# Kernel optimization log

Measured on AMD Instinct MI355X. Metric: run time of the kernel, lower is better.

Reference implementation:

```python
import jax, jax.numpy as jnp
import numpy as np

VOCAB = 100000
EMBED = 256
HIDDEN = 256
HOPS = 3
NHEAD = 4
SEQEND = 2
B, MEM, SEN, QLEN = 32, 50, 20, 20


def setup_inputs() -> dict:
    key = jax.random.key(0)
    ks = jax.random.split(key, 24)

    def lin(k, o, i):
        return jax.random.normal(k, (o, i), jnp.float32) * (1.0 / np.sqrt(i))

    story = jax.random.randint(ks[0], (B, MEM, SEN), 3, VOCAB, dtype=jnp.int32)
    pos_s = jax.random.randint(ks[1], (B, MEM), 0, SEN, dtype=jnp.int32)
    story = jnp.where(jnp.arange(SEN)[None, None, :] == pos_s[..., None], SEQEND, story)
    query = jax.random.randint(ks[2], (B, QLEN), 3, VOCAB, dtype=jnp.int32)
    pos_q = jax.random.randint(ks[3], (B,), 0, QLEN, dtype=jnp.int32)
    query = jnp.where(jnp.arange(QLEN)[None, :] == pos_q[:, None], SEQEND, query)

    embed = jax.random.normal(ks[4], (VOCAB, EMBED), jnp.float32) * 0.05
    embed = embed.at[0].set(0.0)  # padding_idx=0
    H = HIDDEN
    params = dict(
        embed=embed,
        w_ih=lin(ks[5], 3 * H, EMBED), w_hh=lin(ks[6], 3 * H, H),
        b_ih=jnp.zeros((3 * H,), jnp.float32), b_hh=jnp.zeros((3 * H,), jnp.float32),
        ft_w1=lin(ks[7], H, H), ft_b1=jnp.zeros((H,), jnp.float32),
        ft_w2=lin(ks[8], H, H), ft_b2=jnp.zeros((H,), jnp.float32),
        wq=lin(ks[9], H, H), bq=jnp.zeros((H,), jnp.float32),
        wk=lin(ks[10], H, H), bk=jnp.zeros((H,), jnp.float32),
        wv=lin(ks[11], H, H), bv=jnp.zeros((H,), jnp.float32),
        wo=lin(ks[12], H, H), bo=jnp.zeros((H,), jnp.float32),
        g_w1=lin(ks[13], 3 * H, 3 * H), g_b1=jnp.zeros((3 * H,), jnp.float32),
        g_w2=lin(ks[14], 3 * H, 3 * H), g_b2=jnp.zeros((3 * H,), jnp.float32),
        v_w=lin(ks[15], VOCAB, 3 * H),
    )
    return dict(story=story, query=query, **params)


def _gru(x, h0, w_ih, w_hh, b_ih, b_hh):
    # x: [N, T, E], h0: [N, H] -> outputs [N, T, H], final h [N, H]
    def step(h, xt):
        gi = xt @ w_ih.T + b_ih
        gh = h @ w_hh.T + b_hh
        i_r, i_z, i_n = jnp.split(gi, 3, axis=-1)
        h_r, h_z, h_n = jnp.split(gh, 3, axis=-1)
        r = jax.nn.sigmoid(i_r + h_r)
        z = jax.nn.sigmoid(i_z + h_z)
        n = jnp.tanh(i_n + r * h_n)
        h_new = (1.0 - z) * n + z * h
        return h_new, h_new
    h_f, ys = jax.lax.scan(step, h0, jnp.swapaxes(x, 0, 1))
    return jnp.swapaxes(ys, 0, 1), h_f


def _seqend_idx(tokens):
    # first index of SEQEND along last axis, else last position
    is_end = tokens == SEQEND
    idx = jnp.argmax(is_end, axis=-1)
    return jnp.where(is_end.any(axis=-1), idx, tokens.shape[-1] - 1)


def reference(story, query, embed, w_ih, w_hh, b_ih, b_hh, ft_w1, ft_b1, ft_w2, ft_b2,
              wq, bq, wk, bk, wv, bv, wo, bo, g_w1, g_b1, g_w2, g_b2, v_w):
    H, nh = HIDDEN, NHEAD
    dk = H // nh

    def f_t(x):
        return jax.nn.relu(x @ ft_w1.T + ft_b1) @ ft_w2.T + ft_b2

    # --- story encoding: GRU hidden carried ACROSS batch elements (as in torch loop) ---
    story_embs = embed[story]  # [B, MEM, SEN, E]
    def story_step(h, emb_b):
        outs, h_f = _gru(emb_b, h, w_ih, w_hh, b_ih, b_hh)  # [MEM, SEN, H]
        return h_f, outs
    h0 = jnp.zeros((story.shape[1], H), story_embs.dtype)
    _, story_outs = jax.lax.scan(story_step, h0, story_embs)  # [B, MEM, SEN, H]

    s_idx = _seqend_idx(story)  # [B, MEM]
    memory_slots = jnp.take_along_axis(story_outs, s_idx[..., None, None], axis=2)[:, :, 0, :]  # [B, MEM, H]

    # --- query encoding ---
    q_embs = embed[query]  # [B, QLEN, E]
    q_outs, _ = _gru(q_embs, jnp.zeros((query.shape[0], H), q_embs.dtype), w_ih, w_hh, b_ih, b_hh)
    q_idx = _seqend_idx(query)  # [B]
    real_query = jnp.take_along_axis(q_outs, q_idx[:, None, None], axis=1)[:, 0, :]  # [B, H]

    # --- multi-hop attention ---
    def mha(qv, mem):
        b, m, _ = mem.shape
        q = (qv @ wq.T + bq).reshape(b, nh, dk)
        k = (mem @ wk.T + bk).reshape(b, m, nh, dk).transpose(0, 2, 1, 3)
        v = (mem @ wv.T + bv).reshape(b, m, nh, dk).transpose(0, 2, 1, 3)
        scores = jnp.einsum('bhmd,bhd->bhm', k, q) / jnp.sqrt(jnp.float32(dk))
        a = jax.nn.softmax(scores, axis=-1)
        out = jnp.einsum('bhm,bhmd->bhd', a, v).reshape(b, H)
        return out @ wo.T + bo

    o_k = f_t(real_query)
    buffers = []
    for _ in range(HOPS):
        mb = mha(o_k, memory_slots)
        buffers.append(mb)
        o_k = f_t(mb)
    memory_buffers = jnp.stack(buffers, axis=1)  # [B, HOPS, H]

    # --- ReasonModule: pairwise MLP over hops ---
    b, K, _ = memory_buffers.shape
    left = jnp.broadcast_to(memory_buffers[:, None, :, :], (b, K, K, H)).reshape(b, K * K, H)
    right = jnp.broadcast_to(memory_buffers[:, :, None, :], (b, K, K, H)).reshape(b, K * K, H)
    qx = jnp.broadcast_to(real_query[:, None, :], (b, K * K, H))
    combined = jnp.concatenate([left, right, qx], axis=-1)  # [B, K*K, 3H]
    t = jax.nn.relu(combined @ g_w1.T + g_b1) @ g_w2.T + g_b2
    reasoning = jax.nn.relu(t).sum(axis=1)  # [B, 3H]

    return reasoning @ v_w.T  # [B, VOCAB]
```

## Files before the change

kernel.cpp:

```cpp
#include <hip/hip_runtime.h>


#define TPB 256
#define NB    32
#define MEMN  50
#define SEN   20
#define VOC   100000
#define SEQEND_TOK 2
#define NGRU  82
#define NTILE 1530

#define GI_OFF    0
#define KVB_OFF   0
#define MB_OFF    819200
#define T1_OFF    843776
#define T2_OFF    1064960
#define RS_OFF    1286144
#define WTIH_OFF  25067520
#define WTHH_OFF  25264128
#define KVT_OFF   25460736
#define WQT_OFF   25591808
#define WOT_OFF   25657344
#define F1T_OFF   25722880
#define F2T_OFF   25788416
#define G1T_OFF   25853952
#define G2T_OFF   26443776
#define BKV_OFF   27033600
#define IDX_OFF   27034112
#define SLOT_OFF  27035744
#define RQ_OFF    27445344
#define CNT_OFF   27453536

__global__ void k_setup(const float* __restrict__ w_ih, const float* __restrict__ w_hh,
                        const float* __restrict__ wk,  const float* __restrict__ wv,
                        const float* __restrict__ wq,  const float* __restrict__ wo,
                        const float* __restrict__ f1,  const float* __restrict__ f2,
                        const float* __restrict__ g1,  const float* __restrict__ g2,
                        const float* __restrict__ bk,  const float* __restrict__ bv,
                        const int* __restrict__ story, const int* __restrict__ query,
                        float* __restrict__ ws)
{
  int g = blockIdx.x * TPB + threadIdx.x;
  if (g < 196608) { int j = g >> 8, k = g & 255; ws[WTIH_OFF + k*768 + j] = w_ih[g]; return; }
  g -= 196608;
  if (g < 196608) { int j = g >> 8, k = g & 255; ws[WTHH_OFF + k*768 + j] = w_hh[g]; return; }
  g -= 196608;
  if (g < 65536) { int j = g >> 8, k = g & 255; ws[KVT_OFF + k*512 + j] = wk[g]; return; }
  g -= 65536;
  if (g < 65536) { int j = g >> 8, k = g & 255; ws[KVT_OFF + k*512 + 256 + j] = wv[g]; return; }
  g -= 65536;
  if (g < 65536) { int j = g >> 8, k = g & 255; ws[WQT_OFF + k*256 + j] = wq[g]; return; }
  g -= 65536;
  if (g < 65536) { int j = g >> 8, k = g & 255; ws[WOT_OFF + k*256 + j] = wo[g]; return; }
  g -= 65536;
  if (g < 65536) { int j = g >> 8, k = g & 255; ws[F1T_OFF + k*256 + j] = f1[g]; return; }
  g -= 65536;
  if (g < 65536) { int j = g >> 8, k = g & 255; ws[F2T_OFF + k*256 + j] = f2[g]; return; }
  g -= 65536;
  if (g < 589824) { int j = g / 768, k = g - j*768; ws[G1T_OFF + k*768 + j] = g1[g]; return; }
  g -= 589824;
  if (g < 589824) { int j = g / 768, k = g - j*768; ws[G2T_OFF + k*768 + j] = g2[g]; return; }
  g -= 589824;
  if (g < 512) { ws[BKV_OFF + g] = (g < 256) ? bk[g] : bv[g - 256]; return; }
  g -= 512;
  if (g < 1600) {
    const int* st = story + g * SEN;
    int idx = SEN - 1;
    for (int t = 0; t < SEN; ++t) { if (st[t] == SEQEND_TOK) { idx = t; break; } }
    ((int*)(ws + IDX_OFF))[g] = idx;
    return;
  }
  g -= 1600;
  if (g < 32) {
    const int* qt = query + g * SEN;
    int idx = SEN - 1;
    for (int t = 0; t < SEN; ++t) { if (qt[t] == SEQEND_TOK) { idx = t; break; } }
    ((int*)(ws + IDX_OFF))[1600 + g] = idx;
    return;
  }
  g -= 32;
  if (g < 33) ((unsigned int*)(ws + CNT_OFF))[g] = 0u;
}

__global__ __launch_bounds__(1024, 1) void k_fused(
    float* __restrict__ gi,
    const float* __restrict__ w_hh, const float* __restrict__ b_hh,
    const int* __restrict__ idxI,
    const float* __restrict__ wihT, const float* __restrict__ b_ih,
    const int* __restrict__ tokS, const int* __restrict__ tokQ,
    const float* __restrict__ embed,
    float* __restrict__ slot_out, float* __restrict__ rq_out,
    unsigned int* __restrict__ cnt)
{
  __shared__ __align__(16) char smem[114688];
  const int bid = blockIdx.x;
  const int tid = threadIdx.x;

  if (bid >= NGRU) {
    float* At = (float*)smem;
    float* Bt = At + 4224;
    const int tix = bid - NGRU;
    const int mt = tix / 6, nt = tix - mt * 6;
    const int m0 = mt * 128, n0 = nt * 128;
    const int tx = tid & 15, ty = (tid >> 4) & 63;
    float acc[2][8] = {};

    for (int k0 = 0; k0 < 256; k0 += 32) {
      for (int idx = tid; idx < 4096; idx += 1024) {
        int r = idx >> 5, kk = idx & 31;
        int row = m0 + r;
        int tok = (row < 32000) ? tokS[row] : tokQ[row - 32000];
        At[r * 33 + kk] = embed[(size_t)tok * 256 + k0 + kk];
      }
      for (int idx = tid; idx < 4096; idx += 1024) {
        int jj = idx & 127, kk = idx >> 7;
        Bt[jj * 33 + kk] = wihT[(k0 + kk) * 768 + n0 + jj];
      }
      __syncthreads();
#pragma unroll
      for (int kk = 0; kk < 32; ++kk) {
        float a0 = At[ty * 33 + kk], a1 = At[(64 + ty) * 33 + kk];
        float bb[8];
#pragma unroll
        for (int i = 0; i < 8; ++i) bb[i] = Bt[(i * 16 + tx) * 33 + kk];
#pragma unroll
        for (int i = 0; i < 8; ++i) { acc[0][i] += a0 * bb[i]; acc[1][i] += a1 * bb[i]; }
      }
      __syncthreads();
    }
#pragma unroll
    for (int i = 0; i < 2; ++i) {
      int row = m0 + i * 64 + ty;
#pragma unroll
      for (int j2 = 0; j2 < 8; ++j2) {
        int col = n0 + j2 * 16 + tx;
        gi[(size_t)row * 768 + col] = acc[i][j2] + b_ih[col];
      }
    }
    __threadfence();
    __syncthreads();
    if (tid == 0) {
      const int rLo = m0, rHi = m0 + 127;
      const int cLo = (rLo < 32000) ? (rLo / 1000) : 32;
      const int cHi = (rHi < 32000) ? (rHi / 1000) : 32;
      __hip_atomic_fetch_add(&cnt[cLo], 1u, __ATOMIC_RELEASE, __HIP_MEMORY_SCOPE_AGENT);
      if (cHi != cLo)
        __hip_atomic_fetch_add(&cnt[cHi], 1u, __ATOMIC_RELEASE, __HIP_MEMORY_SCOPE_AGENT);
    }
    return;
  }

  const int mode = (bid >= MEMN) ? 1 : 0;
  const int blk = mode ? (bid - MEMN) : bid;
  float* __restrict__ cap_out = mode ? rq_out : slot_out;

  float* tot   = (float*)smem;
  float* ptail = tot + 768;
  float* hs    = ptail + 768;

  float4 w4[48];
  if (tid < 768) {
    const float* wrow = w_hh + (size_t)tid * 256;
#pragma unroll
    for (int q = 0; q < 48; ++q) w4[q] = ((const float4*)wrow)[q];
  } else {
    const int u = tid - 768;
#pragma unroll
    for (int rr = 0; rr < 3; ++rr) {
      const float* wrow = w_hh + (size_t)(u + rr * 256) * 256 + 192;
#pragma unroll
      for (int q = 0; q < 16; ++q) w4[rr * 16 + q] = ((const float4*)wrow)[q];
    }
  }
  const float bh = (tid < 768) ? b_hh[tid] : 0.f;

  if (tid < 256) hs[tid] = 0.f;
  float hold = 0.f;
  __syncthreads();

  const int steps = mode ? SEN : (NB * SEN);
  int b = 0, t = 0, cs = 0;

#pragma unroll 1
  for (int s = 0; s < steps; ++s) {
    if (t == 0) {
      if (tid == 0) {
        const int c   = mode ? 32 : b;
        const int rLo = mode ? 32000 : b * 1000;
        const int rHi = mode ? 32639 : b * 1000 + 999;
        const unsigned expv = 6u * (unsigned)(rHi / 128 - rLo / 128 + 1);
        while (__hip_atomic_load(&cnt[c], __ATOMIC_ACQUIRE, __HIP_MEMORY_SCOPE_AGENT) < expv)
          __builtin_amdgcn_s_sleep(16);
      }
      __syncthreads();
      cs = idxI[mode ? (1600 + blk) : (b * MEMN + blk)];
    }
    const int srow = mode ? (32000 + blk * SEN + t) : (b * 1000 + blk * SEN + t);

    if (tid < 768) {
      float dot = 0.f;
#pragma unroll
      for (int q = 0; q < 48; ++q) {
        float4 h4 = ((const float4*)hs)[q];
        dot += w4[q].x * h4.x + w4[q].y * h4.y + w4[q].z * h4.z + w4[q].w * h4.w;
      }
      float v = dot + bh;
      if (tid < 512) v += gi[(size_t)srow * 768 + tid];
      tot[tid] = v;
    } else {
      const int u = tid - 768;
      float p0 = 0.f, p1 = 0.f, p2 = 0.f;
      const float4* ht = (const float4*)(hs + 192);
#pragma unroll
      for (int q = 0; q < 16; ++q) {
        float4 h4 = ht[q];
        p0 += w4[q     ].x * h4.x + w4[q     ].y * h4.y + w4[q     ].z * h4.z + w4[q     ].w * h4.w;
        p1 += w4[16 + q].x * h4.x + w4[16 + q].y * h4.y + w4[16 + q].z * h4.z + w4[16 + q].w * h4.w;
        p2 += w4[32 + q].x * h4.x + w4[32 + q].y * h4.y + w4[32 + q].z * h4.z + w4[32 + q].w * h4.w;
      }
      ptail[u] = p0; ptail[u + 256] = p1; ptail[u + 512] = p2;
    }
    __syncthreads();

    if (tid < 256) {
      float Sr = tot[tid]       + ptail[tid];
      float Sz = tot[tid + 256] + ptail[tid + 256];
      float Sn = tot[tid + 512] + ptail[tid + 512];
      float gn = gi[(size_t)srow * 768 + 512 + tid];
      float rg = 1.f / (1.f + __expf(-Sr));
      float zg = 1.f / (1.f + __expf(-Sz));
      float xn = gn + rg * Sn;
      xn = fminf(fmaxf(xn, -15.f), 15.f);
      float e2 = __expf(-2.f * xn);
      float ng = (1.f - e2) / (1.f + e2);
      float hnew = (1.f - zg) * ng + zg * hold;
      hs[tid] = hnew;
      if (t == cs) cap_out[(mode ? blk : (b * MEMN + blk)) * 256 + tid] = hnew;
      hold = hnew;
    }
    __syncthreads();
    if (++t == SEN) { t = 0; ++b; }
  }
}

template<int MODE, int BM>
__global__ __launch_bounds__(256) void k_gemm(
    const float* __restrict__ A, const float* __restrict__ B,
    const float* __restrict__ bias, float* __restrict__ C,
    int M, int N, int K, int relu,
    const float* __restrict__ mbp, const float* __restrict__ rqp)
{
  __shared__ float At[BM * 33];
  __shared__ float Bt[128 * 33];
  constexpr int R = BM / 16;
  const int m0 = blockIdx.x * BM, n0 = blockIdx.y * 128;
  const int tx = threadIdx.x & 15, ty = threadIdx.x >> 4;
  float acc[R][8] = {};

  for (int k0 = 0; k0 < K; k0 += 32) {
    for (int idx = threadIdx.x; idx < BM * 32; idx += 256) {
      int r = idx >> 5, kk = idx & 31;
      int row = m0 + r, kg = k0 + kk;
      float v = 0.f;
      if (MODE == 2) {
        if (row < 288) {
          int b = row / 9, p = row - b * 9;
          v = (kg < 256) ? mbp[(b*3 + (p % 3))*256 + kg]
            : (kg < 512) ? mbp[(b*3 + (p / 3))*256 + (kg - 256)]
                         : rqp[b*256 + (kg - 512)];
        }
      } else {
        if (row < M) v = A[(size_t)row * K + kg];
      }
      At[r * 33 + kk] = v;
    }
    for (int idx = threadIdx.x; idx < 4096; idx += 256) {
      int jj = idx & 127, kk = idx >> 7;
      Bt[jj * 33 + kk] = B[(k0 + kk) * N + n0 + jj];
    }
    __syncthreads();
#pragma unroll
    for (int kk = 0; kk < 32; ++kk) {
      float a[R], bb[8];
#pragma unroll
      for (int i = 0; i < R; ++i) a[i] = At[(i * 16 + ty) * 33 + kk];
#pragma unroll
      for (int i = 0; i < 8; ++i) bb[i] = Bt[(i * 16 + tx) * 33 + kk];
#pragma unroll
      for (int i = 0; i < R; ++i)
#pragma unroll
        for (int j2 = 0; j2 < 8; ++j2) acc[i][j2] += a[i] * bb[j2];
    }
    __syncthreads();
  }
#pragma unroll
  for (int i = 0; i < R; ++i) {
    int row = m0 + i * 16 + ty;
    if (row >= M) continue;
#pragma unroll
    for (int j2 = 0; j2 < 8; ++j2) {
      int col = n0 + j2 * 16 + tx;
      float v = acc[i][j2] + bias[col];
      if (relu) v = fmaxf(v, 0.f);
      C[(size_t)row * N + col] = v;
    }
  }
}

__device__ __forceinline__ float gemv256(const float* __restrict__ WT,
                                         const float* __restrict__ xs, int j)
{
  float acc = 0.f;
#pragma unroll 64
  for (int k = 0; k < 256; ++k) acc += xs[k] * WT[k * 256 + j];
  return acc;
}

__global__ __launch_bounds__(256) void k_hops(
    const float* __restrict__ rq, const float* __restrict__ kvb,
    const float* __restrict__ wqT, const float* __restrict__ bq,
    const float* __restrict__ woT, const float* __restrict__ bo,
    const float* __restrict__ f1T, const float* __restrict__ fb1,
    const float* __restrict__ f2T, const float* __restrict__ fb2,
    float* __restrict__ mb)
{
  const int b = blockIdx.x, j = threadIdx.x;
  __shared__ float lk[50 * 259];
  __shared__ float lv[50 * 259];
  __shared__ float xs[256], tb[256], qs[256], avs[256], ob[256], asc[256];

  for (int idx = j; idx < 12800; idx += 256) {
    int m = idx >> 8, d = idx & 255;
    lk[m * 259 + d] = kvb[(b * MEMN + m) * 512 + d];
    lv[m * 259 + d] = kvb[(b * MEMN + m) * 512 + 256 + d];
  }
  xs[j] = rq[b * 256 + j];
  __syncthreads();

  float v = fmaxf(gemv256(f1T, xs, j) + fb1[j], 0.f);
  __syncthreads(); tb[j] = v; __syncthreads();
  v = gemv256(f2T, tb, j) + fb2[j];
  __syncthreads(); xs[j] = v; __syncthreads();

  for (int hop = 0; hop < 3; ++hop) {
    v = gemv256(wqT, xs, j) + bq[j];
    __syncthreads(); qs[j] = v; __syncthreads();

    const int w = j >> 6, l = j & 63;
    float sc = -1e30f;
    if (l < MEMN) {
      sc = 0.f;
#pragma unroll 16
      for (int d = 0; d < 64; ++d) sc += qs[w * 64 + d] * lk[l * 259 + w * 64 + d];
      sc *= 0.125f;
    }
    float mx = sc;
#pragma unroll
    for (int off = 32; off > 0; off >>= 1) mx = fmaxf(mx, __shfl_xor(mx, off));
    float e = (l < MEMN) ? __expf(sc - mx) : 0.f;
    float sm = e;
#pragma unroll
    for (int off = 32; off > 0; off >>= 1) sm += __shfl_xor(sm, off);
    float a = e / sm;
    __syncthreads(); asc[j] = a; __syncthreads();

    float av = 0.f;
#pragma unroll 10
    for (int m = 0; m < MEMN; ++m) av += asc[w * 64 + m] * lv[m * 259 + w * 64 + l];
    __syncthreads(); avs[j] = av; __syncthreads();

    v = gemv256(woT, avs, j) + bo[j];
    mb[(b * 3 + hop) * 256 + j] = v;
    if (hop < 2) {
      __syncthreads(); ob[j] = v; __syncthreads();
      v = fmaxf(gemv256(f1T, ob, j) + fb1[j], 0.f);
      __syncthreads(); tb[j] = v; __syncthreads();
      v = gemv256(f2T, tb, j) + fb2[j];
      __syncthreads(); xs[j] = v; __syncthreads();
    }
  }
}

__global__ void k_rsum(const float* __restrict__ t2, float* __restrict__ rs)
{
  int gid = blockIdx.x * TPB + threadIdx.x;
  int b = gid / 768, jj = gid - b * 768;
  float acc = 0.f;
#pragma unroll
  for (int p = 0; p < 9; ++p) acc += t2[(b * 9 + p) * 768 + jj];
  rs[b * 768 + jj] = acc;
}

__global__ __launch_bounds__(256) void k_vocab(const float* __restrict__ rs,
                                               const float* __restrict__ vw,
                                               float* __restrict__ out)
{
  __shared__ float vt[64 * 132];
  __shared__ float rt[32 * 132];
  const int c0 = blockIdx.x * 64;
  const int tx = threadIdx.x & 15, ty = threadIdx.x >> 4;
  float acc[2][4] = {{0.f,0.f,0.f,0.f},{0.f,0.f,0.f,0.f}};

  for (int k0 = 0; k0 < 768; k0 += 128) {
    for (int idx = threadIdx.x; idx < 2048; idx += 256) {
      int r = idx >> 5, q = idx & 31;
      int col = c0 + r;
      float4 v4 = make_float4(0.f, 0.f, 0.f, 0.f);
      if (col < VOC) v4 = ((const float4*)(vw + (size_t)col * 768 + k0))[q];
      *(float4*)&vt[r * 132 + q * 4] = v4;
    }
    for (int idx = threadIdx.x; idx < 1024; idx += 256) {
      int r = idx >> 5, q = idx & 31;
      float4 v4 = ((const float4*)(rs + r * 768 + k0))[q];
      *(float4*)&rt[r * 132 + q * 4] = v4;
    }
    __syncthreads();
#pragma unroll 4
    for (int kk = 0; kk < 128; ++kk) {
      float a0 = rt[(ty * 2 + 0) * 132 + kk];
      float a1 = rt[(ty * 2 + 1) * 132 + kk];
#pragma unroll
      for (int cc = 0; cc < 4; ++cc) {
        float bv_ = vt[(tx + cc * 16) * 132 + kk];
        acc[0][cc] += a0 * bv_;
        acc[1][cc] += a1 * bv_;
      }
    }
    __syncthreads();
  }
#pragma unroll
  for (int rr = 0; rr < 2; ++rr)
#pragma unroll
    for (int cc = 0; cc < 4; ++cc) {
      int c = c0 + tx + cc * 16;
      if (c < VOC) out[(ty * 2 + rr) * VOC + c] = acc[rr][cc];
    }
}

extern "C" void kernel_launch(void* const* d_in, const int* in_sizes, int n_in,
                              void* d_out, int out_size, void* d_ws, size_t ws_size,
                              hipStream_t stream)
{
  const int*   story = (const int*)d_in[0];
  const int*   query = (const int*)d_in[1];
  const float* embed = (const float*)d_in[2];
  const float* w_ih  = (const float*)d_in[3];
  const float* w_hh  = (const float*)d_in[4];
  const float* b_ih  = (const float*)d_in[5];
  const float* b_hh  = (const float*)d_in[6];
  const float* ft_w1 = (const float*)d_in[7];
  const float* ft_b1 = (const float*)d_in[8];
  const float* ft_w2 = (const float*)d_in[9];
  const float* ft_b2 = (const float*)d_in[10];
  const float* wq    = (const float*)d_in[11];
  const float* bq    = (const float*)d_in[12];
  const float* wk    = (const float*)d_in[13];
  const float* bk    = (const float*)d_in[14];
  const float* wv    = (const float*)d_in[15];
  const float* bv    = (const float*)d_in[16];
  const float* wo    = (const float*)d_in[17];
  const float* bo    = (const float*)d_in[18];
  const float* g_w1  = (const float*)d_in[19];
  const float* g_b1  = (const float*)d_in[20];
  const float* g_w2  = (const float*)d_in[21];
  const float* g_b2  = (const float*)d_in[22];
  const float* v_w   = (const float*)d_in[23];
  float* out = (float*)d_out;
  float* ws  = (float*)d_ws;

  k_setup<<<7689, TPB, 0, stream>>>(w_ih, w_hh, wk, wv, wq, wo, ft_w1, ft_w2,
                                    g_w1, g_w2, bk, bv, story, query, ws);
  k_fused<<<NGRU + NTILE, 1024, 0, stream>>>(
      ws + GI_OFF, w_hh, b_hh, (const int*)(ws + IDX_OFF),
      ws + WTIH_OFF, b_ih, story, query, embed,
      ws + SLOT_OFF, ws + RQ_OFF, (unsigned int*)(ws + CNT_OFF));
  k_gemm<0,128><<<dim3(13, 4), TPB, 0, stream>>>(
      ws + SLOT_OFF, ws + KVT_OFF, ws + BKV_OFF, ws + KVB_OFF, 1600, 512, 256, 0,
      nullptr, nullptr);
  k_hops<<<NB, TPB, 0, stream>>>(ws + RQ_OFF, ws + KVB_OFF,
                                 ws + WQT_OFF, bq, ws + WOT_OFF, bo,
                                 ws + F1T_OFF, ft_b1, ws + F2T_OFF, ft_b2,
                                 ws + MB_OFF);
  k_gemm<2,32><<<dim3(9, 6), TPB, 0, stream>>>(
      nullptr, ws + G1T_OFF, g_b1, ws + T1_OFF, 288, 768, 768, 1,
      ws + MB_OFF, ws + RQ_OFF);
  k_gemm<0,32><<<dim3(9, 6), TPB, 0, stream>>>(
      ws + T1_OFF, ws + G2T_OFF, g_b2, ws + T2_OFF, 288, 768, 768, 1,
      nullptr, nullptr);
  k_rsum<<<96, TPB, 0, stream>>>(ws + T2_OFF, ws + RS_OFF);
  k_vocab<<<(VOC + 63) / 64, TPB, 0, stream>>>(ws + RS_OFF, v_w, out);
}
```

Measured before the change: 9.359 ms.

## Split each GRU recurrence across four cooperating blocks with inter-block sync

Replaces the fused input-projection plus GRU kernel with a separate embedding-gather GEMM and a new GRU kernel. The GRU kernel runs each memory-slot chain across four blocks, each holding a 192-row slice of the transposed hidden weights in registers. Per step, partial gate sums go to global memory and the blocks synchronise through atomic counters. This spreads the serial recurrence over more CUs and shortens per-step compute, at the cost of a global-memory round trip and a spin barrier on every timestep, and it drops the overlap the fused kernel had between projection and recurrence.

```diff
diff --git a/kernel.cpp b/kernel.cpp
--- a/kernel.cpp
+++ b/kernel.cpp
@@ -7,8 +7,9 @@
 #define SEN   20
 #define VOC   100000
 #define SEQEND_TOK 2
-#define NGRU  82
-#define NTILE 1530
+#define GBLK  4
+#define GTHR  768
+#define GROWS 192
 
 #define GI_OFF    0
 #define KVB_OFF   0
@@ -29,7 +30,9 @@
 #define IDX_OFF   27034112
 #define SLOT_OFF  27035744
 #define RQ_OFF    27445344
-#define CNT_OFF   27453536
+#define G_OFF     27453536
+#define GQ_OFF    27530336
+#define SCNT_OFF  27579488
 
 __global__ void k_setup(const float* __restrict__ w_ih, const float* __restrict__ w_hh,
                         const float* __restrict__ wk,  const float* __restrict__ wv,
@@ -79,168 +82,7 @@
     return;
   }
   g -= 32;
-  if (g < 33) ((unsigned int*)(ws + CNT_OFF))[g] = 0u;
-}
-
-__global__ __launch_bounds__(1024, 1) void k_fused(
-    float* __restrict__ gi,
-    const float* __restrict__ w_hh, const float* __restrict__ b_hh,
-    const int* __restrict__ idxI,
-    const float* __restrict__ wihT, const float* __restrict__ b_ih,
-    const int* __restrict__ tokS, const int* __restrict__ tokQ,
-    const float* __restrict__ embed,
-    float* __restrict__ slot_out, float* __restrict__ rq_out,
-    unsigned int* __restrict__ cnt)
-{
-  __shared__ __align__(16) char smem[114688];
-  const int bid = blockIdx.x;
-  const int tid = threadIdx.x;
-
-  if (bid >= NGRU) {
-    float* At = (float*)smem;
-    float* Bt = At + 4224;
-    const int tix = bid - NGRU;
-    const int mt = tix / 6, nt = tix - mt * 6;
-    const int m0 = mt * 128, n0 = nt * 128;
-    const int tx = tid & 15, ty = (tid >> 4) & 63;
-    float acc[2][8] = {};
-
-    for (int k0 = 0; k0 < 256; k0 += 32) {
-      for (int idx = tid; idx < 4096; idx += 1024) {
-        int r = idx >> 5, kk = idx & 31;
-        int row = m0 + r;
-        int tok = (row < 32000) ? tokS[row] : tokQ[row - 32000];
-        At[r * 33 + kk] = embed[(size_t)tok * 256 + k0 + kk];
-      }
-      for (int idx = tid; idx < 4096; idx += 1024) {
-        int jj = idx & 127, kk = idx >> 7;
-        Bt[jj * 33 + kk] = wihT[(k0 + kk) * 768 + n0 + jj];
-      }
-      __syncthreads();
-#pragma unroll
-      for (int kk = 0; kk < 32; ++kk) {
-        float a0 = At[ty * 33 + kk], a1 = At[(64 + ty) * 33 + kk];
-        float bb[8];
-#pragma unroll
-        for (int i = 0; i < 8; ++i) bb[i] = Bt[(i * 16 + tx) * 33 + kk];
-#pragma unroll
-        for (int i = 0; i < 8; ++i) { acc[0][i] += a0 * bb[i]; acc[1][i] += a1 * bb[i]; }
-      }
-      __syncthreads();
-    }
-#pragma unroll
-    for (int i = 0; i < 2; ++i) {
-      int row = m0 + i * 64 + ty;
-#pragma unroll
-      for (int j2 = 0; j2 < 8; ++j2) {
-        int col = n0 + j2 * 16 + tx;
-        gi[(size_t)row * 768 + col] = acc[i][j2] + b_ih[col];
-      }
-    }
-    __threadfence();
-    __syncthreads();
-    if (tid == 0) {
-      const int rLo = m0, rHi = m0 + 127;
-      const int cLo = (rLo < 32000) ? (rLo / 1000) : 32;
-      const int cHi = (rHi < 32000) ? (rHi / 1000) : 32;
-      __hip_atomic_fetch_add(&cnt[cLo], 1u, __ATOMIC_RELEASE, __HIP_MEMORY_SCOPE_AGENT);
-      if (cHi != cLo)
-        __hip_atomic_fetch_add(&cnt[cHi], 1u, __ATOMIC_RELEASE, __HIP_MEMORY_SCOPE_AGENT);
-    }
-    return;
-  }
-
-  const int mode = (bid >= MEMN) ? 1 : 0;
-  const int blk = mode ? (bid - MEMN) : bid;
-  float* __restrict__ cap_out = mode ? rq_out : slot_out;
-
-  float* tot   = (float*)smem;
-  float* ptail = tot + 768;
-  float* hs    = ptail + 768;
-
-  float4 w4[48];
-  if (tid < 768) {
-    const float* wrow = w_hh + (size_t)tid * 256;
-#pragma unroll
-    for (int q = 0; q < 48; ++q) w4[q] = ((const float4*)wrow)[q];
-  } else {
-    const int u = tid - 768;
-#pragma unroll
-    for (int rr = 0; rr < 3; ++rr) {
-      const float* wrow = w_hh + (size_t)(u + rr * 256) * 256 + 192;
-#pragma unroll
-      for (int q = 0; q < 16; ++q) w4[rr * 16 + q] = ((const float4*)wrow)[q];
-    }
-  }
-  const float bh = (tid < 768) ? b_hh[tid] : 0.f;
-
-  if (tid < 256) hs[tid] = 0.f;
-  float hold = 0.f;
-  __syncthreads();
-
-  const int steps = mode ? SEN : (NB * SEN);
-  int b = 0, t = 0, cs = 0;
-
-#pragma unroll 1
-  for (int s = 0; s < steps; ++s) {
-    if (t == 0) {
-      if (tid == 0) {
-        const int c   = mode ? 32 : b;
-        const int rLo = mode ? 32000 : b * 1000;
-        const int rHi = mode ? 32639 : b * 1000 + 999;
-        const unsigned expv = 6u * (unsigned)(rHi / 128 - rLo / 128 + 1);
-        while (__hip_atomic_load(&cnt[c], __ATOMIC_ACQUIRE, __HIP_MEMORY_SCOPE_AGENT) < expv)
-          __builtin_amdgcn_s_sleep(16);
-      }
-      __syncthreads();
-      cs = idxI[mode ? (1600 + blk) : (b * MEMN + blk)];
-    }
-    const int srow = mode ? (32000 + blk * SEN + t) : (b * 1000 + blk * SEN + t);
-
-    if (tid < 768) {
-      float dot = 0.f;
-#pragma unroll
-      for (int q = 0; q < 48; ++q) {
-        float4 h4 = ((const float4*)hs)[q];
-        dot += w4[q].x * h4.x + w4[q].y * h4.y + w4[q].z * h4.z + w4[q].w * h4.w;
-      }
-      float v = dot + bh;
-      if (tid < 512) v += gi[(size_t)srow * 768 + tid];
-      tot[tid] = v;
-    } else {
-      const int u = tid - 768;
-      float p0 = 0.f, p1 = 0.f, p2 = 0.f;
-      const float4* ht = (const float4*)(hs + 192);
-#pragma unroll
-      for (int q = 0; q < 16; ++q) {
-        float4 h4 = ht[q];
-        p0 += w4[q     ].x * h4.x + w4[q     ].y * h4.y + w4[q     ].z * h4.z + w4[q     ].w * h4.w;
-        p1 += w4[16 + q].x * h4.x + w4[16 + q].y * h4.y + w4[16 + q].z * h4.z + w4[16 + q].w * h4.w;
-        p2 += w4[32 + q].x * h4.x + w4[32 + q].y * h4.y + w4[32 + q].z * h4.z + w4[32 + q].w * h4.w;
-      }
-      ptail[u] = p0; ptail[u + 256] = p1; ptail[u + 512] = p2;
-    }
-    __syncthreads();
-
-    if (tid < 256) {
-      float Sr = tot[tid]       + ptail[tid];
-      float Sz = tot[tid + 256] + ptail[tid + 256];
-      float Sn = tot[tid + 512] + ptail[tid + 512];
-      float gn = gi[(size_t)srow * 768 + 512 + tid];
-      float rg = 1.f / (1.f + __expf(-Sr));
-      float zg = 1.f / (1.f + __expf(-Sz));
-      float xn = gn + rg * Sn;
-      xn = fminf(fmaxf(xn, -15.f), 15.f);
-      float e2 = __expf(-2.f * xn);
-      float ng = (1.f - e2) / (1.f + e2);
-      float hnew = (1.f - zg) * ng + zg * hold;
-      hs[tid] = hnew;
-      if (t == cs) cap_out[(mode ? blk : (b * MEMN + blk)) * 256 + tid] = hnew;
-      hold = hnew;
-    }
-    __syncthreads();
-    if (++t == SEN) { t = 0; ++b; }
-  }
+  if (g < 82) ((unsigned int*)(ws + SCNT_OFF))[g] = 0u;
 }
 
 template<int MODE, int BM>
@@ -248,6 +90,8 @@
     const float* __restrict__ A, const float* __restrict__ B,
     const float* __restrict__ bias, float* __restrict__ C,
     int M, int N, int K, int relu,
+    const int* __restrict__ tokS, const int* __restrict__ tokQ,
+    const float* __restrict__ embed,
     const float* __restrict__ mbp, const float* __restrict__ rqp)
 {
   __shared__ float At[BM * 33];
@@ -262,7 +106,10 @@
       int r = idx >> 5, kk = idx & 31;
       int row = m0 + r, kg = k0 + kk;
       float v = 0.f;
-      if (MODE == 2) {
+      if (MODE == 1) {
+        int tok = (row < 32000) ? tokS[row] : tokQ[row - 32000];
+        v = embed[(size_t)tok * 256 + kg];
+      } else if (MODE == 2) {
         if (row < 288) {
           int b = row / 9, p = row - b * 9;
           v = (kg < 256) ? mbp[(b*3 + (p % 3))*256 + kg]
@@ -307,6 +154,174 @@
   }
 }
 
+__global__ __launch_bounds__(GTHR, 1) void k_gru(
+    const float* __restrict__ gi, const float* __restrict__ wT,
+    const float* __restrict__ b_hh, const int* __restrict__ idxI,
+    float* __restrict__ slot_out, float* __restrict__ rq_out,
+    float* __restrict__ G, float* __restrict__ GQ,
+    unsigned int* __restrict__ scnt, unsigned int* __restrict__ qcnt)
+{
+  __shared__ __align__(16) float smem[24576];
+  float* hs     = smem;
+  float* part   = smem + 256;
+  float* st_own = smem + 1024;
+  float* st_gn  = smem + 4864;
+
+  const int c = blockIdx.x / GBLK;
+  const int p = blockIdx.x - c * GBLK;
+  const int rowbase = p * GROWS;
+  const int tid = threadIdx.x;
+  const int q = tid / GROWS;
+  const int r = tid - q * GROWS;
+  const int grow = rowbase + r;
+
+  float4 wv[16];
+#pragma unroll
+  for (int i = 0; i < 16; ++i) {
+    const int col = q * 64 + 4 * i;
+    wv[i].x = wT[(col + 0) * 768 + grow];
+    wv[i].y = wT[(col + 1) * 768 + grow];
+    wv[i].z = wT[(col + 2) * 768 + grow];
+    wv[i].w = wT[(col + 3) * 768 + grow];
+  }
+#pragma unroll
+  for (int i = 0; i < 16; ++i)
+    asm volatile("" : "+v"(wv[i].x), "+v"(wv[i].y), "+v"(wv[i].z), "+v"(wv[i].w));
+  const float bh = b_hh[grow];
+
+  float hold = 0.f;
+  if (tid < 256) hs[tid] = 0.f;
+  float* Gc = G + c * 1536;
+  unsigned sigma = 0;
+
+  for (int b = 0; b < NB; ++b) {
+    __syncthreads();
+    const int srow0 = b * 1000 + c * SEN;
+    for (int idx = tid; idx < SEN * 256; idx += GTHR) {
+      const int tt = idx >> 8, d = idx & 255;
+      st_gn[idx] = gi[(size_t)(srow0 + tt) * 768 + 512 + d];
+    }
+    if (rowbase < 512) {
+      for (int idx = tid; idx < SEN * GROWS; idx += GTHR) {
+        const int tt = idx / GROWS, d = idx - tt * GROWS;
+        const int gg = rowbase + d;
+        st_own[idx] = (gg < 512) ? gi[(size_t)(srow0 + tt) * 768 + gg] : 0.f;
+      }
+    }
+    const int cs = idxI[b * MEMN + c];
+    __syncthreads();
+
+    for (int t = 0; t < SEN; ++t) {
+      ++sigma;
+      const float4* h4p = (const float4*)hs + q * 16;
+      float dot = 0.f;
+#pragma unroll
+      for (int i = 0; i < 16; ++i) {
+        float4 h4 = h4p[i];
+        dot += wv[i].x*h4.x + wv[i].y*h4.y + wv[i].z*h4.z + wv[i].w*h4.w;
+      }
+      part[tid] = dot;
+      __syncthreads();
+      if (tid < GROWS) {
+        float S = part[tid] + part[GROWS+tid] + part[2*GROWS+tid] + part[3*GROWS+tid] + bh;
+        if (grow < 512) S += st_own[t*GROWS+tid];
+        Gc[(sigma & 1) * 768 + rowbase + tid] = S;
+      }
+      __threadfence();
+      __syncthreads();
+      if (tid == 0) {
+        __hip_atomic_fetch_add(&scnt[c], 1u, __ATOMIC_RELEASE, __HIP_MEMORY_SCOPE_AGENT);
+        while (__hip_atomic_load(&scnt[c], __ATOMIC_ACQUIRE, __HIP_MEMORY_SCOPE_AGENT) < (unsigned)GBLK * sigma)
+          __builtin_amdgcn_s_sleep(1);
+      }
+      __syncthreads();
+      if (tid < 256) {
+        const float* gb = Gc + (sigma & 1) * 768;
+        float Sr = __hip_atomic_load(gb + tid,       __ATOMIC_RELAXED, __HIP_MEMORY_SCOPE_AGENT);
+        float Sz = __hip_atomic_load(gb + 256 + tid, __ATOMIC_RELAXED, __HIP_MEMORY_SCOPE_AGENT);
+        float Sn = __hip_atomic_load(gb + 512 + tid, __ATOMIC_RELAXED, __HIP_MEMORY_SCOPE_AGENT);
+        float gn = st_gn[t*256+tid];
+        float rg = 1.f / (1.f + __expf(-Sr));
+        float zg = 1.f / (1.f + __expf(-Sz));
+        float xn = gn + rg * Sn;
+        xn = fminf(fmaxf(xn, -15.f), 15.f);
+        float e2 = __expf(-2.f * xn);
+        float ng = (1.f - e2) / (1.f + e2);
+        float hnew = (1.f - zg) * ng + zg * hold;
+        hold = hnew;
+        hs[tid] = hnew;
+        if (t == cs && p == 0) slot_out[(b * MEMN + c) * 256 + tid] = hnew;
+      }
+      __syncthreads();
+    }
+  }
+
+  if (c < NB) {
+    __syncthreads();
+    hold = 0.f;
+    if (tid < 256) hs[tid] = 0.f;
+    const int srow0 = 32000 + c * SEN;
+    for (int idx = tid; idx < SEN * 256; idx += GTHR) {
+      const int tt = idx >> 8, d = idx & 255;
+      st_gn[idx] = gi[(size_t)(srow0 + tt) * 768 + 512 + d];
+    }
+    if (rowbase < 512) {
+      for (int idx = tid; idx < SEN * GROWS; idx += GTHR) {
+        const int tt = idx / GROWS, d = idx - tt * GROWS;
+        const int gg = rowbase + d;
+        st_own[idx] = (gg < 512) ? gi[(size_t)(srow0 + tt) * 768 + gg] : 0.f;
+      }
+    }
+    const int cs = idxI[1600 + c];
+    float* Gq = GQ + c * 1536;
+    __syncthreads();
+    unsigned sq = 0;
+    for (int t = 0; t < SEN; ++t) {
+      ++sq;
+      const float4* h4p = (const float4*)hs + q * 16;
+      float dot = 0.f;
+#pragma unroll
+      for (int i = 0; i < 16; ++i) {
+        float4 h4 = h4p[i];
+        dot += wv[i].x*h4.x + wv[i].y*h4.y + wv[i].z*h4.z + wv[i].w*h4.w;
+      }
+      part[tid] = dot;
+      __syncthreads();
+      if (tid < GROWS) {
+        float S = part[tid] + part[GROWS+tid] + part[2*GROWS+tid] + part[3*GROWS+tid] + bh;
+        if (grow < 512) S += st_own[t*GROWS+tid];
+        Gq[(sq & 1) * 768 + rowbase + tid] = S;
+      }
+      __threadfence();
+      __syncthreads();
+      if (tid == 0) {
+        __hip_atomic_fetch_add(&qcnt[c], 1u, __ATOMIC_RELEASE, __HIP_MEMORY_SCOPE_AGENT);
+        while (__hip_atomic_load(&qcnt[c], __ATOMIC_ACQUIRE, __HIP_MEMORY_SCOPE_AGENT) < (unsigned)GBLK * sq)
+          __builtin_amdgcn_s_sleep(1);
+      }
+      __syncthreads();
+      if (tid < 256) {
+        const float* gb = Gq + (sq & 1) * 768;
+        float Sr = __hip_atomic_load(gb + tid,       __ATOMIC_RELAXED, __HIP_MEMORY_SCOPE_AGENT);
+        float Sz = __hip_atomic_load(gb + 256 + tid, __ATOMIC_RELAXED, __HIP_MEMORY_SCOPE_AGENT);
+        float Sn = __hip_atomic_load(gb + 512 + tid, __ATOMIC_RELAXED, __HIP_MEMORY_SCOPE_AGENT);
+        float gn = st_gn[t*256+tid];
+        float rg = 1.f / (1.f + __expf(-Sr));
+        float zg = 1.f / (1.f + __expf(-Sz));
+        float xn = gn + rg * Sn;
+        xn = fminf(fmaxf(xn, -15.f), 15.f);
+        float e2 = __expf(-2.f * xn);
+        float ng = (1.f - e2) / (1.f + e2);
+        float hnew = (1.f - zg) * ng + zg * hold;
+        hold = hnew;
+        hs[tid] = hnew;
+        if (t == cs && p == 0) rq_out[c * 256 + tid] = hnew;
+      }
+      __syncthreads();
+    }
+  }
+}
+
 __device__ __forceinline__ float gemv256(const float* __restrict__ WT,
                                          const float* __restrict__ xs, int j)
 {
@@ -432,8 +447,8 @@
   for (int rr = 0; rr < 2; ++rr)
 #pragma unroll
     for (int cc = 0; cc < 4; ++cc) {
-      int c = c0 + tx + cc * 16;
-      if (c < VOC) out[(ty * 2 + rr) * VOC + c] = acc[rr][cc];
+      int cx = c0 + tx + cc * 16;
+      if (cx < VOC) out[(ty * 2 + rr) * VOC + cx] = acc[rr][cc];
     }
 }
 
@@ -470,23 +485,26 @@
 
   k_setup<<<7689, TPB, 0, stream>>>(w_ih, w_hh, wk, wv, wq, wo, ft_w1, ft_w2,
                                     g_w1, g_w2, bk, bv, story, query, ws);
-  k_fused<<<NGRU + NTILE, 1024, 0, stream>>>(
-      ws + GI_OFF, w_hh, b_hh, (const int*)(ws + IDX_OFF),
-      ws + WTIH_OFF, b_ih, story, query, embed,
-      ws + SLOT_OFF, ws + RQ_OFF, (unsigned int*)(ws + CNT_OFF));
+  k_gemm<1,128><<<dim3(255, 6), TPB, 0, stream>>>(
+      nullptr, ws + WTIH_OFF, b_ih, ws + GI_OFF, 32640, 768, 256, 0,
+      story, query, embed, nullptr, nullptr);
+  k_gru<<<MEMN * GBLK, GTHR, 0, stream>>>(
+      ws + GI_OFF, ws + WTHH_OFF, b_hh, (const int*)(ws + IDX_OFF),
+      ws + SLOT_OFF, ws + RQ_OFF, ws + G_OFF, ws + GQ_OFF,
+      (unsigned int*)(ws + SCNT_OFF), (unsigned int*)(ws + SCNT_OFF) + 50);
   k_gemm<0,128><<<dim3(13, 4), TPB, 0, stream>>>(
       ws + SLOT_OFF, ws + KVT_OFF, ws + BKV_OFF, ws + KVB_OFF, 1600, 512, 256, 0,
-      nullptr, nullptr);
+      nullptr, nullptr, nullptr, nullptr, nullptr);
   k_hops<<<NB, TPB, 0, stream>>>(ws + RQ_OFF, ws + KVB_OFF,
                                  ws + WQT_OFF, bq, ws + WOT_OFF, bo,
                                  ws + F1T_OFF, ft_b1, ws + F2T_OFF, ft_b2,
                                  ws + MB_OFF);
   k_gemm<2,32><<<dim3(9, 6), TPB, 0, stream>>>(
       nullptr, ws + G1T_OFF, g_b1, ws + T1_OFF, 288, 768, 768, 1,
-      ws + MB_OFF, ws + RQ_OFF);
+      nullptr, nullptr, nullptr, ws + MB_OFF, ws + RQ_OFF);
   k_gemm<0,32><<<dim3(9, 6), TPB, 0, stream>>>(
       ws + T1_OFF, ws + G2T_OFF, g_b2, ws + T2_OFF, 288, 768, 768, 1,
-      nullptr, nullptr);
+      nullptr, nullptr, nullptr, nullptr, nullptr);
   k_rsum<<<96, TPB, 0, stream>>>(ws + T2_OFF, ws + RS_OFF);
   k_vocab<<<(VOC + 63) / 64, TPB, 0, stream>>>(ws + RS_OFF, v_w, out);
 }
```

After: 30.41 ms. +225.0%, slower.
